# Kernel optimization log

Measured on AMD Instinct MI355X. Metric: run time of the kernel, lower is better.

## Reference

```python
import jax, jax.numpy as jnp
import numpy as np

B, N, D_POINTS, D_MODEL = 2, 65536, 64, 128
SCALE = 1.0 / np.float32(np.sqrt(D_MODEL))


def setup_inputs() -> dict:
    key = jax.random.key(0)
    ks = jax.random.split(key, 20)
    def lin(k, fan_in, fan_out):
        s = 1.0 / np.sqrt(fan_in)
        return jax.random.uniform(k, (fan_in, fan_out), jnp.float32, -s, s)
    return {
        "xyz": jax.random.normal(ks[0], (B, N, 3), jnp.float32),
        "features": jax.random.normal(ks[1], (B, N, D_POINTS), jnp.float32),
        "fc1_w": lin(ks[2], D_POINTS, D_MODEL), "fc1_b": jnp.zeros((D_MODEL,), jnp.float32),
        "fc2_w": lin(ks[3], D_MODEL, D_POINTS), "fc2_b": jnp.zeros((D_POINTS,), jnp.float32),
        "d1_w": lin(ks[4], 3, D_MODEL), "d1_b": jnp.zeros((D_MODEL,), jnp.float32),
        "d2_w": lin(ks[5], D_MODEL, D_MODEL), "d2_b": jnp.zeros((D_MODEL,), jnp.float32),
        "g1_w": lin(ks[6], D_MODEL, D_MODEL), "g1_b": jnp.zeros((D_MODEL,), jnp.float32),
        "g2_w": lin(ks[7], D_MODEL, D_MODEL), "g2_b": jnp.zeros((D_MODEL,), jnp.float32),
        "wq": lin(ks[8], D_MODEL, D_MODEL),
        "wk": lin(ks[9], D_MODEL, D_MODEL),
        "wv": lin(ks[10], D_MODEL, D_MODEL),
    }


def reference(xyz, features, fc1_w, fc1_b, fc2_w, fc2_b, d1_w, d1_b, d2_w, d2_b,
              g1_w, g1_b, g2_w, g2_b, wq, wk, wv):
    # x: [B, N, d_model]
    x = features @ fc1_w + fc1_b
    q = x @ wq
    k = x @ wk
    v = x @ wv
    # position encoding MLP on xyz: [B, N, d_model]
    pos_enc = jax.nn.relu(xyz @ d1_w + d1_b) @ d2_w + d2_b
    # vector attention: elementwise q - k + pos_enc, gamma MLP, per-channel softmax over points
    attn = jax.nn.relu((q - k + pos_enc) @ g1_w + g1_b) @ g2_w + g2_b
    attn = jax.nn.softmax(attn * SCALE, axis=-2)  # softmax over N (point axis)
    # elementwise gating of values
    res = attn * (v + pos_enc)
    res = res @ fc2_w + fc2_b + features  # residual
    return (res, attn)
```

## Files before the change

### kernel.cpp

```cpp
#include <hip/hip_runtime.h>
#include <hip/hip_bf16.h>

#define BB 2
#define NN 65536
#define DP 64
#define DM 128
#define SCALEF 0.08838834764831845f

typedef __attribute__((ext_vector_type(8))) short short8v;
typedef __attribute__((ext_vector_type(4))) float float4v;

__device__ __forceinline__ unsigned short f2bf(float f) {
  unsigned u = __float_as_uint(f);
  u += 0x7FFFu + ((u >> 16) & 1u);
  return (unsigned short)(u >> 16);
}
__device__ __forceinline__ float bf2f(unsigned short h) {
  return __uint_as_float(((unsigned)h) << 16);
}

__global__ __launch_bounds__(256) void k0_kernel(
    const float* __restrict__ wq, const float* __restrict__ wk,
    const float* __restrict__ fc1_w, const float* __restrict__ fc2_w,
    const float* __restrict__ d2_w, const float* __restrict__ g1_w,
    const float* __restrict__ g2_w, const float* __restrict__ wv_w,
    float* __restrict__ sums,
    short* __restrict__ d2t, short* __restrict__ fc1t, short* __restrict__ wqkt,
    short* __restrict__ g1t, short* __restrict__ g2t, short* __restrict__ wvt,
    short* __restrict__ fc2t) {
  int t = threadIdx.x, bi = blockIdx.x;
  if (bi == 0) sums[t] = 0.f;
  int mat = bi >> 5, blk = bi & 31;
  if (mat == 1) {
    int i = blk * 256 + t;
    int n = i >> 6, k = i & 63;
    fc1t[n * 64 + k] = (short)f2bf(fc1_w[k * 128 + n]);
  } else if (mat == 6) {
    int i = blk * 256 + t;
    int n = i >> 7, k = i & 127;
    fc2t[n * 128 + k] = (short)f2bf(fc2_w[k * 64 + n]);
  } else {
    const float* src = (mat == 0) ? d2_w : (mat == 2) ? wq : (mat == 3) ? g1_w
                     : (mat == 4) ? g2_w : wv_w;
    short* dst = (mat == 0) ? d2t : (mat == 2) ? wqkt : (mat == 3) ? g1t
               : (mat == 4) ? g2t : wvt;
#pragma unroll
    for (int j = 0; j < 2; ++j) {
      int i = blk * 512 + t + j * 256;
      int n = i >> 7, k = i & 127;
      float v = src[k * 128 + n];
      if (mat == 2) v -= wk[k * 128 + n];
      dst[n * 128 + k] = (short)f2bf(v);
    }
  }
}

template<int K>
__device__ __forceinline__ void loadB(const short* __restrict__ Wt,
                                      int wid, int col, int quad, short8v b[2][4]) {
#pragma unroll
  for (int nt = 0; nt < 2; ++nt)
#pragma unroll
    for (int kt = 0; kt < K / 32; ++kt)
      b[nt][kt] = *(const short8v*)(Wt + (wid * 32 + nt * 16 + col) * K + kt * 32 + quad * 8);
}

template<int K>
__device__ __forceinline__ void gemm_compute(const short* __restrict__ A,
                                             const short8v b[2][4],
                                             int col, int quad, float4v acc[2][2]) {
#pragma unroll
  for (int kt = 0; kt < K / 32; ++kt) {
#pragma unroll
    for (int mt = 0; mt < 2; ++mt) {
      short8v a = *(const short8v*)(A + (mt * 16 + col) * 136 + kt * 32 + quad * 8);
      acc[mt][0] = __builtin_amdgcn_mfma_f32_16x16x32_bf16(a, b[0][kt], acc[mt][0], 0, 0, 0);
      acc[mt][1] = __builtin_amdgcn_mfma_f32_16x16x32_bf16(a, b[1][kt], acc[mt][1], 0, 0, 0);
    }
  }
}

__device__ __forceinline__ void store_tile(short* __restrict__ dst,
                                           const float4v acc[2][2],
                                           int wid, int col, int quad,
                                           float b0, float b1, bool do_relu) {
#pragma unroll
  for (int mt = 0; mt < 2; ++mt)
#pragma unroll
    for (int nt = 0; nt < 2; ++nt) {
      float bias = nt ? b1 : b0;
#pragma unroll
      for (int r = 0; r < 4; ++r) {
        float v = acc[mt][nt][r] + bias;
        if (do_relu) v = fmaxf(v, 0.f);
        dst[(mt * 16 + quad * 4 + r) * 136 + wid * 32 + nt * 16 + col] = (short)f2bf(v);
      }
    }
}

#define ZERO_ACC(acc) \
  _Pragma("unroll") for (int mt = 0; mt < 2; ++mt) \
  _Pragma("unroll") for (int nt = 0; nt < 2; ++nt) \
  _Pragma("unroll") for (int r = 0; r < 4; ++r) acc[mt][nt][r] = 0.f;

__global__ __launch_bounds__(256, 5) void k1_kernel(
    const float* __restrict__ xyz, const float* __restrict__ features,
    const short* __restrict__ fc1t, const float* __restrict__ fc1_b,
    const float* __restrict__ d1_w, const float* __restrict__ d1_b,
    const short* __restrict__ d2t, const float* __restrict__ d2_b,
    const short* __restrict__ g1t, const float* __restrict__ g1_b,
    const short* __restrict__ g2t, const float* __restrict__ g2_b,
    const short* __restrict__ wqkt, const short* __restrict__ wvt,
    unsigned short* __restrict__ Ebf, unsigned short* __restrict__ Gbf,
    float* __restrict__ sums) {
  __shared__ __align__(16) short As[32 * 136];
  __shared__ __align__(16) short Xs[32 * 136];

  const int tid = threadIdx.x;
  const int wid = tid >> 6, lane = tid & 63;
  const int col = lane & 15, quad = lane >> 4;
  const long long p0 = (long long)blockIdx.x * 32;
  const int bi = (int)(p0 >> 16);

  short8v b[2][4];
  loadB<128>(d2t, wid, col, quad, b);

  float* xf = (float*)Xs;
  if (tid < 96) xf[tid] = xyz[p0 * 3 + tid];
  __syncthreads();

  {
    const int tn = tid & 31, tm = tid >> 5;
    const int c4 = tn * 4, pbase = tm * 4;
    float4 w0 = *(const float4*)(d1_w + c4);
    float4 w1 = *(const float4*)(d1_w + 128 + c4);
    float4 w2 = *(const float4*)(d1_w + 256 + c4);
    float4 bb = *(const float4*)(d1_b + c4);
#pragma unroll
    for (int p = 0; p < 4; ++p) {
      float x0 = xf[(pbase + p) * 3 + 0];
      float x1 = xf[(pbase + p) * 3 + 1];
      float x2 = xf[(pbase + p) * 3 + 2];
      short4 rr;
      rr.x = (short)f2bf(fmaxf(0.f, fmaf(x0, w0.x, fmaf(x1, w1.x, fmaf(x2, w2.x, bb.x)))));
      rr.y = (short)f2bf(fmaxf(0.f, fmaf(x0, w0.y, fmaf(x1, w1.y, fmaf(x2, w2.y, bb.y)))));
      rr.z = (short)f2bf(fmaxf(0.f, fmaf(x0, w0.z, fmaf(x1, w1.z, fmaf(x2, w2.z, bb.z)))));
      rr.w = (short)f2bf(fmaxf(0.f, fmaf(x0, w0.w, fmaf(x1, w1.w, fmaf(x2, w2.w, bb.w)))));
      *(short4*)(As + (pbase + p) * 136 + c4) = rr;
    }
  }
  __syncthreads();

  const int ch0 = wid * 32 + col, ch1 = ch0 + 16;
  float4v pe[2][2], acc[2][2];

  ZERO_ACC(acc)
  gemm_compute<128>(As, b, col, quad, acc);
  {
    float b0 = d2_b[ch0], b1 = d2_b[ch1];
#pragma unroll
    for (int mt = 0; mt < 2; ++mt)
#pragma unroll
      for (int r = 0; r < 4; ++r) {
        pe[mt][0][r] = acc[mt][0][r] + b0;
        pe[mt][1][r] = acc[mt][1][r] + b1;
      }
  }
  loadB<64>(fc1t, wid, col, quad, b);
  __syncthreads();

#pragma unroll
  for (int j = 0; j < 2; ++j) {
    int c = tid + j * 256;
    float4 f = *(const float4*)(features + p0 * 64 + (long long)c * 4);
    int row = c >> 4, cp = (c & 15) * 4;
    short4 s;
    s.x = (short)f2bf(f.x); s.y = (short)f2bf(f.y);
    s.z = (short)f2bf(f.z); s.w = (short)f2bf(f.w);
    *(short4*)(As + row * 136 + cp) = s;
  }
  __syncthreads();

  ZERO_ACC(acc)
  gemm_compute<64>(As, b, col, quad, acc);
  store_tile(Xs, acc, wid, col, quad, fc1_b[ch0], fc1_b[ch1], false);
  loadB<128>(wqkt, wid, col, quad, b);
  __syncthreads();

#pragma unroll
  for (int mt = 0; mt < 2; ++mt)
#pragma unroll
    for (int nt = 0; nt < 2; ++nt)
#pragma unroll
      for (int r = 0; r < 4; ++r) acc[mt][nt][r] = pe[mt][nt][r];
  gemm_compute<128>(Xs, b, col, quad, acc);
  store_tile(As, acc, wid, col, quad, 0.f, 0.f, false);
  loadB<128>(g1t, wid, col, quad, b);
  __syncthreads();

  ZERO_ACC(acc)
  gemm_compute<128>(As, b, col, quad, acc);
  __syncthreads();
  store_tile(As, acc, wid, col, quad, g1_b[ch0], g1_b[ch1], true);
  loadB<128>(g2t, wid, col, quad, b);
  __syncthreads();

  ZERO_ACC(acc)
  gemm_compute<128>(As, b, col, quad, acc);
  {
    short8v b2[2][4];
    loadB<128>(wvt, wid, col, quad, b2);
    float b0 = g2_b[ch0], b1 = g2_b[ch1];
    float s0 = 0.f, s1 = 0.f;
#pragma unroll
    for (int mt = 0; mt < 2; ++mt)
#pragma unroll
      for (int r = 0; r < 4; ++r) {
        long long row = p0 + mt * 16 + quad * 4 + r;
        float e0 = __expf((acc[mt][0][r] + b0) * SCALEF);
        float e1 = __expf((acc[mt][1][r] + b1) * SCALEF);
        Ebf[row * DM + ch0] = f2bf(e0);
        Ebf[row * DM + ch1] = f2bf(e1);
        s0 += e0; s1 += e1;
      }
    s0 += __shfl_xor(s0, 16, 64); s0 += __shfl_xor(s0, 32, 64);
    s1 += __shfl_xor(s1, 16, 64); s1 += __shfl_xor(s1, 32, 64);
    if (quad == 0) {
      atomicAdd(&sums[bi * DM + ch0], s0);
      atomicAdd(&sums[bi * DM + ch1], s1);
    }

#pragma unroll
    for (int mt = 0; mt < 2; ++mt)
#pragma unroll
      for (int nt = 0; nt < 2; ++nt)
#pragma unroll
        for (int r = 0; r < 4; ++r) acc[mt][nt][r] = pe[mt][nt][r];
    gemm_compute<128>(Xs, b2, col, quad, acc);
#pragma unroll
    for (int mt = 0; mt < 2; ++mt)
#pragma unroll
      for (int r = 0; r < 4; ++r) {
        long long row = p0 + mt * 16 + quad * 4 + r;
        Gbf[row * DM + ch0] = f2bf(acc[mt][0][r]);
        Gbf[row * DM + ch1] = f2bf(acc[mt][1][r]);
      }
  }
}

__global__ __launch_bounds__(256, 5) void k3_kernel(
    const unsigned short* __restrict__ Ebf, float* __restrict__ out_attn,
    float* __restrict__ out_res, const unsigned short* __restrict__ Gbf,
    const float* __restrict__ sums,
    const short* __restrict__ fc2t, const float* __restrict__ fc2_b,
    const float* __restrict__ features) {
  __shared__ __align__(16) short Ys[32 * 136];
  const int tid = threadIdx.x;
  const long long p0 = (long long)blockIdx.x * 32;
  const int bi = (int)(p0 >> 16);

  {
    const int tn = tid & 15, tm = tid >> 4;
    const int c8 = tn * 8;
    float4 sv0 = *(const float4*)(sums + bi * DM + c8);
    float4 sv1 = *(const float4*)(sums + bi * DM + c8 + 4);
    float4 r0, r1;
    r0.x = 1.f / sv0.x; r0.y = 1.f / sv0.y; r0.z = 1.f / sv0.z; r0.w = 1.f / sv0.w;
    r1.x = 1.f / sv1.x; r1.y = 1.f / sv1.y; r1.z = 1.f / sv1.z; r1.w = 1.f / sv1.w;
#pragma unroll
    for (int it = 0; it < 2; ++it) {
      int row = tm + it * 16;
      long long idx = (p0 + row) * DM + c8;
      short8v e8 = *(const short8v*)(Ebf + idx);
      short8v g8 = *(const short8v*)(Gbf + idx);
      float a[8];
      a[0] = bf2f((unsigned short)e8[0]) * r0.x; a[1] = bf2f((unsigned short)e8[1]) * r0.y;
      a[2] = bf2f((unsigned short)e8[2]) * r0.z; a[3] = bf2f((unsigned short)e8[3]) * r0.w;
      a[4] = bf2f((unsigned short)e8[4]) * r1.x; a[5] = bf2f((unsigned short)e8[5]) * r1.y;
      a[6] = bf2f((unsigned short)e8[6]) * r1.z; a[7] = bf2f((unsigned short)e8[7]) * r1.w;
      float4 a0 = {a[0], a[1], a[2], a[3]};
      float4 a1 = {a[4], a[5], a[6], a[7]};
      *(float4*)(out_attn + idx) = a0;
      *(float4*)(out_attn + idx + 4) = a1;
      short8v y;
#pragma unroll
      for (int q = 0; q < 8; ++q)
        y[q] = (short)f2bf(a[q] * bf2f((unsigned short)g8[q]));
      *(short8v*)(Ys + row * 136 + c8) = y;
    }
  }

  const int wid = tid >> 6, lane = tid & 63;
  const int col = lane & 15, quad = lane >> 4;
  const int n = wid * 16 + col;
  short8v bw[4];
#pragma unroll
  for (int kt = 0; kt < 4; ++kt)
    bw[kt] = *(const short8v*)(fc2t + n * DM + kt * 32 + quad * 8);
  __syncthreads();

  float4v acc[2];
#pragma unroll
  for (int mt = 0; mt < 2; ++mt)
#pragma unroll
    for (int r = 0; r < 4; ++r) acc[mt][r] = 0.f;
#pragma unroll
  for (int kt = 0; kt < 4; ++kt)
#pragma unroll
    for (int mt = 0; mt < 2; ++mt) {
      short8v a = *(const short8v*)(Ys + (mt * 16 + col) * 136 + kt * 32 + quad * 8);
      acc[mt] = __builtin_amdgcn_mfma_f32_16x16x32_bf16(a, bw[kt], acc[mt], 0, 0, 0);
    }
  __syncthreads();
  float* yf = (float*)Ys;
  float bb = fc2_b[n];
#pragma unroll
  for (int mt = 0; mt < 2; ++mt)
#pragma unroll
    for (int r = 0; r < 4; ++r)
      yf[(mt * 16 + quad * 4 + r) * 68 + n] = acc[mt][r] + bb;
  __syncthreads();

#pragma unroll
  for (int it = 0; it < 2; ++it) {
    int idx = tid + it * 256;
    int row = idx >> 4, ch = idx & 15;
    float4 v = *(const float4*)(yf + row * 68 + ch * 4);
    float4 ft = *(const float4*)(features + (p0 + row) * DP + ch * 4);
    float4 o;
    o.x = v.x + ft.x; o.y = v.y + ft.y; o.z = v.z + ft.z; o.w = v.w + ft.w;
    *(float4*)(out_res + (p0 + row) * DP + ch * 4) = o;
  }
}

extern "C" void kernel_launch(void* const* d_in, const int* in_sizes, int n_in,
                              void* d_out, int out_size, void* d_ws, size_t ws_size,
                              hipStream_t stream) {
  const float* xyz      = (const float*)d_in[0];
  const float* features = (const float*)d_in[1];
  const float* fc1_w    = (const float*)d_in[2];
  const float* fc1_b    = (const float*)d_in[3];
  const float* fc2_w    = (const float*)d_in[4];
  const float* fc2_b    = (const float*)d_in[5];
  const float* d1_w     = (const float*)d_in[6];
  const float* d1_b     = (const float*)d_in[7];
  const float* d2_w     = (const float*)d_in[8];
  const float* d2_b     = (const float*)d_in[9];
  const float* g1_w     = (const float*)d_in[10];
  const float* g1_b     = (const float*)d_in[11];
  const float* g2_w     = (const float*)d_in[12];
  const float* g2_b     = (const float*)d_in[13];
  const float* wq       = (const float*)d_in[14];
  const float* wk       = (const float*)d_in[15];
  const float* wv       = (const float*)d_in[16];

  float* out_res  = (float*)d_out;
  float* out_attn = out_res + (long long)BB * NN * DP;

  float* sums = (float*)d_ws;
  short* d2t  = (short*)(sums + 256);
  short* fc1t = d2t + 16384;
  short* wqkt = fc1t + 8192;
  short* g1t  = wqkt + 16384;
  short* g2t  = g1t + 16384;
  short* wvt  = g2t + 16384;
  short* fc2t = wvt + 16384;
  unsigned short* Ebf = (unsigned short*)(fc2t + 8192);
  unsigned short* Gbf = (unsigned short*)d_out;

  hipLaunchKernelGGL(k0_kernel, dim3(224), dim3(256), 0, stream,
                     wq, wk, fc1_w, fc2_w, d2_w, g1_w, g2_w, wv,
                     sums, d2t, fc1t, wqkt, g1t, g2t, wvt, fc2t);
  hipLaunchKernelGGL(k1_kernel, dim3((BB * NN) / 32), dim3(256), 0, stream,
                     xyz, features, fc1t, fc1_b, d1_w, d1_b, d2t, d2_b,
                     g1t, g1_b, g2t, g2_b, wqkt, wvt, Ebf, Gbf, sums);
  hipLaunchKernelGGL(k3_kernel, dim3((BB * NN) / 32), dim3(256), 0, stream,
                     Ebf, out_attn, out_res, Gbf, sums, fc2t, fc2_b, features);
}
```

Measured before the change: 283.9 us.

## Make k1/k3 persistent with register-resident weights and batched softmax-sum atomics

Both point-wise kernels go from one 32-point tile per block to 512 blocks that each loop over 8 consecutive tiles. All B-operand weight fragments, biases and softmax reciprocals are loaded once per block and kept in registers, and the softmax partial sums are accumulated across iterations so atomics happen once per block. Global loads of features and xyz are issued at the top of each iteration ahead of the barriers to overlap latency. The cost is much higher register pressure (five 128x128 weight fragment sets held at once, launch bounds lowered to 2) and only 512 blocks, which may limit occupancy and latency hiding on a 256-CU part.

```diff
diff --git a/kernel.cpp b/kernel.cpp
--- a/kernel.cpp
+++ b/kernel.cpp
@@ -9,6 +9,11 @@
 
 typedef __attribute__((ext_vector_type(8))) short short8v;
 typedef __attribute__((ext_vector_type(4))) float float4v;
+
+#define K1_GRID 512
+#define K1_ITERS 8
+#define K3_GRID 512
+#define K3_ITERS 8
 
 __device__ __forceinline__ unsigned short f2bf(float f) {
   unsigned u = __float_as_uint(f);
@@ -103,7 +108,12 @@
   _Pragma("unroll") for (int nt = 0; nt < 2; ++nt) \
   _Pragma("unroll") for (int r = 0; r < 4; ++r) acc[mt][nt][r] = 0.f;
 
-__global__ __launch_bounds__(256, 5) void k1_kernel(
+#define COPY_ACC(dst, src) \
+  _Pragma("unroll") for (int mt = 0; mt < 2; ++mt) \
+  _Pragma("unroll") for (int nt = 0; nt < 2; ++nt) \
+  _Pragma("unroll") for (int r = 0; r < 4; ++r) dst[mt][nt][r] = src[mt][nt][r];
+
+__global__ __launch_bounds__(256, 2) void k1_kernel(
     const float* __restrict__ xyz, const float* __restrict__ features,
     const short* __restrict__ fc1t, const float* __restrict__ fc1_b,
     const float* __restrict__ d1_w, const float* __restrict__ d1_b,
@@ -119,124 +129,119 @@
   const int tid = threadIdx.x;
   const int wid = tid >> 6, lane = tid & 63;
   const int col = lane & 15, quad = lane >> 4;
-  const long long p0 = (long long)blockIdx.x * 32;
-  const int bi = (int)(p0 >> 16);
-
-  short8v b[2][4];
-  loadB<128>(d2t, wid, col, quad, b);
-
+  const int bk = blockIdx.x;
+  const int bi = bk >> 8;
+  const int ch0 = wid * 32 + col, ch1 = ch0 + 16;
+
+  short8v Bd2[2][4], Bqk[2][4], Bg1[2][4], Bg2[2][4], Bwv[2][4];
+  loadB<128>(d2t, wid, col, quad, Bd2);
+  loadB<128>(wqkt, wid, col, quad, Bqk);
+  loadB<128>(g1t, wid, col, quad, Bg1);
+  loadB<128>(g2t, wid, col, quad, Bg2);
+  loadB<128>(wvt, wid, col, quad, Bwv);
+
+  const float d2b0 = d2_b[ch0], d2b1 = d2_b[ch1];
+  const float f1b0 = fc1_b[ch0], f1b1 = fc1_b[ch1];
+  const float g1b0 = g1_b[ch0], g1b1 = g1_b[ch1];
+  const float g2b0 = g2_b[ch0], g2b1 = g2_b[ch1];
+
+  float s0 = 0.f, s1 = 0.f;
   float* xf = (float*)Xs;
-  if (tid < 96) xf[tid] = xyz[p0 * 3 + tid];
-  __syncthreads();
-
-  {
-    const int tn = tid & 31, tm = tid >> 5;
-    const int c4 = tn * 4, pbase = tm * 4;
-    float4 w0 = *(const float4*)(d1_w + c4);
-    float4 w1 = *(const float4*)(d1_w + 128 + c4);
-    float4 w2 = *(const float4*)(d1_w + 256 + c4);
-    float4 bb = *(const float4*)(d1_b + c4);
-#pragma unroll
-    for (int p = 0; p < 4; ++p) {
-      float x0 = xf[(pbase + p) * 3 + 0];
-      float x1 = xf[(pbase + p) * 3 + 1];
-      float x2 = xf[(pbase + p) * 3 + 2];
-      short4 rr;
-      rr.x = (short)f2bf(fmaxf(0.f, fmaf(x0, w0.x, fmaf(x1, w1.x, fmaf(x2, w2.x, bb.x)))));
-      rr.y = (short)f2bf(fmaxf(0.f, fmaf(x0, w0.y, fmaf(x1, w1.y, fmaf(x2, w2.y, bb.y)))));
-      rr.z = (short)f2bf(fmaxf(0.f, fmaf(x0, w0.z, fmaf(x1, w1.z, fmaf(x2, w2.z, bb.z)))));
-      rr.w = (short)f2bf(fmaxf(0.f, fmaf(x0, w0.w, fmaf(x1, w1.w, fmaf(x2, w2.w, bb.w)))));
-      *(short4*)(As + (pbase + p) * 136 + c4) = rr;
-    }
-  }
-  __syncthreads();
-
-  const int ch0 = wid * 32 + col, ch1 = ch0 + 16;
-  float4v pe[2][2], acc[2][2];
-
-  ZERO_ACC(acc)
-  gemm_compute<128>(As, b, col, quad, acc);
-  {
-    float b0 = d2_b[ch0], b1 = d2_b[ch1];
+
+  for (int it = 0; it < K1_ITERS; ++it) {
+    const long long p0 = ((long long)bk * K1_ITERS + it) * 32;
+
+    float xr = 0.f;
+    if (tid < 96) xr = xyz[p0 * 3 + tid];
+    float4 f0 = *(const float4*)(features + p0 * 64 + (long long)tid * 4);
+    float4 f1 = *(const float4*)(features + p0 * 64 + (long long)(tid + 256) * 4);
+    short8v Bf1[2][4];
+    loadB<64>(fc1t, wid, col, quad, Bf1);
+
+    __syncthreads();
+    if (tid < 96) xf[tid] = xr;
+    __syncthreads();
+
+    {
+      const int tn = tid & 31, tm = tid >> 5;
+      const int c4 = tn * 4, pbase = tm * 4;
+      float4 w0 = *(const float4*)(d1_w + c4);
+      float4 w1 = *(const float4*)(d1_w + 128 + c4);
+      float4 w2 = *(const float4*)(d1_w + 256 + c4);
+      float4 bb = *(const float4*)(d1_b + c4);
+#pragma unroll
+      for (int p = 0; p < 4; ++p) {
+        float x0 = xf[(pbase + p) * 3 + 0];
+        float x1 = xf[(pbase + p) * 3 + 1];
+        float x2 = xf[(pbase + p) * 3 + 2];
+        short4 rr;
+        rr.x = (short)f2bf(fmaxf(0.f, fmaf(x0, w0.x, fmaf(x1, w1.x, fmaf(x2, w2.x, bb.x)))));
+        rr.y = (short)f2bf(fmaxf(0.f, fmaf(x0, w0.y, fmaf(x1, w1.y, fmaf(x2, w2.y, bb.y)))));
+        rr.z = (short)f2bf(fmaxf(0.f, fmaf(x0, w0.z, fmaf(x1, w1.z, fmaf(x2, w2.z, bb.z)))));
+        rr.w = (short)f2bf(fmaxf(0.f, fmaf(x0, w0.w, fmaf(x1, w1.w, fmaf(x2, w2.w, bb.w)))));
+        *(short4*)(As + (pbase + p) * 136 + c4) = rr;
+      }
+    }
+    __syncthreads();
+
+    float4v pe[2][2], acc[2][2];
+
+    ZERO_ACC(acc)
+    gemm_compute<128>(As, Bd2, col, quad, acc);
 #pragma unroll
     for (int mt = 0; mt < 2; ++mt)
 #pragma unroll
       for (int r = 0; r < 4; ++r) {
-        pe[mt][0][r] = acc[mt][0][r] + b0;
-        pe[mt][1][r] = acc[mt][1][r] + b1;
-      }
-  }
-  loadB<64>(fc1t, wid, col, quad, b);
-  __syncthreads();
-
-#pragma unroll
-  for (int j = 0; j < 2; ++j) {
-    int c = tid + j * 256;
-    float4 f = *(const float4*)(features + p0 * 64 + (long long)c * 4);
-    int row = c >> 4, cp = (c & 15) * 4;
-    short4 s;
-    s.x = (short)f2bf(f.x); s.y = (short)f2bf(f.y);
-    s.z = (short)f2bf(f.z); s.w = (short)f2bf(f.w);
-    *(short4*)(As + row * 136 + cp) = s;
-  }
-  __syncthreads();
-
-  ZERO_ACC(acc)
-  gemm_compute<64>(As, b, col, quad, acc);
-  store_tile(Xs, acc, wid, col, quad, fc1_b[ch0], fc1_b[ch1], false);
-  loadB<128>(wqkt, wid, col, quad, b);
-  __syncthreads();
-
-#pragma unroll
-  for (int mt = 0; mt < 2; ++mt)
-#pragma unroll
-    for (int nt = 0; nt < 2; ++nt)
-#pragma unroll
-      for (int r = 0; r < 4; ++r) acc[mt][nt][r] = pe[mt][nt][r];
-  gemm_compute<128>(Xs, b, col, quad, acc);
-  store_tile(As, acc, wid, col, quad, 0.f, 0.f, false);
-  loadB<128>(g1t, wid, col, quad, b);
-  __syncthreads();
-
-  ZERO_ACC(acc)
-  gemm_compute<128>(As, b, col, quad, acc);
-  __syncthreads();
-  store_tile(As, acc, wid, col, quad, g1_b[ch0], g1_b[ch1], true);
-  loadB<128>(g2t, wid, col, quad, b);
-  __syncthreads();
-
-  ZERO_ACC(acc)
-  gemm_compute<128>(As, b, col, quad, acc);
-  {
-    short8v b2[2][4];
-    loadB<128>(wvt, wid, col, quad, b2);
-    float b0 = g2_b[ch0], b1 = g2_b[ch1];
-    float s0 = 0.f, s1 = 0.f;
+        pe[mt][0][r] = acc[mt][0][r] + d2b0;
+        pe[mt][1][r] = acc[mt][1][r] + d2b1;
+      }
+    __syncthreads();
+
+    {
+      int c = tid, row = c >> 4, cp = (c & 15) * 4;
+      short4 s;
+      s.x = (short)f2bf(f0.x); s.y = (short)f2bf(f0.y);
+      s.z = (short)f2bf(f0.z); s.w = (short)f2bf(f0.w);
+      *(short4*)(As + row * 136 + cp) = s;
+      c = tid + 256; row = c >> 4; cp = (c & 15) * 4;
+      s.x = (short)f2bf(f1.x); s.y = (short)f2bf(f1.y);
+      s.z = (short)f2bf(f1.z); s.w = (short)f2bf(f1.w);
+      *(short4*)(As + row * 136 + cp) = s;
+    }
+    __syncthreads();
+
+    ZERO_ACC(acc)
+    gemm_compute<64>(As, Bf1, col, quad, acc);
+    store_tile(Xs, acc, wid, col, quad, f1b0, f1b1, false);
+    __syncthreads();
+
+    COPY_ACC(acc, pe)
+    gemm_compute<128>(Xs, Bqk, col, quad, acc);
+    store_tile(As, acc, wid, col, quad, 0.f, 0.f, false);
+    __syncthreads();
+
+    ZERO_ACC(acc)
+    gemm_compute<128>(As, Bg1, col, quad, acc);
+    __syncthreads();
+    store_tile(As, acc, wid, col, quad, g1b0, g1b1, true);
+    __syncthreads();
+
+    ZERO_ACC(acc)
+    gemm_compute<128>(As, Bg2, col, quad, acc);
 #pragma unroll
     for (int mt = 0; mt < 2; ++mt)
 #pragma unroll
       for (int r = 0; r < 4; ++r) {
         long long row = p0 + mt * 16 + quad * 4 + r;
-        float e0 = __expf((acc[mt][0][r] + b0) * SCALEF);
-        float e1 = __expf((acc[mt][1][r] + b1) * SCALEF);
+        float e0 = __expf((acc[mt][0][r] + g2b0) * SCALEF);
+        float e1 = __expf((acc[mt][1][r] + g2b1) * SCALEF);
         Ebf[row * DM + ch0] = f2bf(e0);
         Ebf[row * DM + ch1] = f2bf(e1);
         s0 += e0; s1 += e1;
       }
-    s0 += __shfl_xor(s0, 16, 64); s0 += __shfl_xor(s0, 32, 64);
-    s1 += __shfl_xor(s1, 16, 64); s1 += __shfl_xor(s1, 32, 64);
-    if (quad == 0) {
-      atomicAdd(&sums[bi * DM + ch0], s0);
-      atomicAdd(&sums[bi * DM + ch1], s1);
-    }
-
-#pragma unroll
-    for (int mt = 0; mt < 2; ++mt)
-#pragma unroll
-      for (int nt = 0; nt < 2; ++nt)
-#pragma unroll
-        for (int r = 0; r < 4; ++r) acc[mt][nt][r] = pe[mt][nt][r];
-    gemm_compute<128>(Xs, b2, col, quad, acc);
+
+    COPY_ACC(acc, pe)
+    gemm_compute<128>(Xs, Bwv, col, quad, acc);
 #pragma unroll
     for (int mt = 0; mt < 2; ++mt)
 #pragma unroll
@@ -246,9 +251,16 @@
         Gbf[row * DM + ch1] = f2bf(acc[mt][1][r]);
       }
   }
-}
-
-__global__ __launch_bounds__(256, 5) void k3_kernel(
+
+  s0 += __shfl_xor(s0, 16, 64); s0 += __shfl_xor(s0, 32, 64);
+  s1 += __shfl_xor(s1, 16, 64); s1 += __shfl_xor(s1, 32, 64);
+  if (quad == 0) {
+    atomicAdd(&sums[bi * DM + ch0], s0);
+    atomicAdd(&sums[bi * DM + ch1], s1);
+  }
+}
+
+__global__ __launch_bounds__(256, 2) void k3_kernel(
     const unsigned short* __restrict__ Ebf, float* __restrict__ out_attn,
     float* __restrict__ out_res, const unsigned short* __restrict__ Gbf,
     const float* __restrict__ sums,
@@ -256,20 +268,39 @@
     const float* __restrict__ features) {
   __shared__ __align__(16) short Ys[32 * 136];
   const int tid = threadIdx.x;
-  const long long p0 = (long long)blockIdx.x * 32;
-  const int bi = (int)(p0 >> 16);
-
-  {
-    const int tn = tid & 15, tm = tid >> 4;
-    const int c8 = tn * 8;
-    float4 sv0 = *(const float4*)(sums + bi * DM + c8);
-    float4 sv1 = *(const float4*)(sums + bi * DM + c8 + 4);
-    float4 r0, r1;
-    r0.x = 1.f / sv0.x; r0.y = 1.f / sv0.y; r0.z = 1.f / sv0.z; r0.w = 1.f / sv0.w;
-    r1.x = 1.f / sv1.x; r1.y = 1.f / sv1.y; r1.z = 1.f / sv1.z; r1.w = 1.f / sv1.w;
-#pragma unroll
-    for (int it = 0; it < 2; ++it) {
-      int row = tm + it * 16;
+  const int bk = blockIdx.x;
+  const int bi = bk >> 8;
+
+  const int wid = tid >> 6, lane = tid & 63;
+  const int col = lane & 15, quad = lane >> 4;
+  const int n = wid * 16 + col;
+  short8v bw[4];
+#pragma unroll
+  for (int kt = 0; kt < 4; ++kt)
+    bw[kt] = *(const short8v*)(fc2t + n * DM + kt * 32 + quad * 8);
+  const float bb = fc2_b[n];
+
+  const int tn = tid & 15, tm = tid >> 4;
+  const int c8 = tn * 8;
+  float4 sv0 = *(const float4*)(sums + bi * DM + c8);
+  float4 sv1 = *(const float4*)(sums + bi * DM + c8 + 4);
+  float4 r0, r1;
+  r0.x = 1.f / sv0.x; r0.y = 1.f / sv0.y; r0.z = 1.f / sv0.z; r0.w = 1.f / sv0.w;
+  r1.x = 1.f / sv1.x; r1.y = 1.f / sv1.y; r1.z = 1.f / sv1.z; r1.w = 1.f / sv1.w;
+
+  for (int it = 0; it < K3_ITERS; ++it) {
+    const long long p0 = ((long long)bk * K3_ITERS + it) * 32;
+
+    int fidx = tid, frow = fidx >> 4, fch = fidx & 15;
+    float4 ft0 = *(const float4*)(features + (p0 + frow) * DP + fch * 4);
+    int fidx1 = tid + 256, frow1 = fidx1 >> 4, fch1 = fidx1 & 15;
+    float4 ft1 = *(const float4*)(features + (p0 + frow1) * DP + fch1 * 4);
+
+    __syncthreads();
+
+#pragma unroll
+    for (int it2 = 0; it2 < 2; ++it2) {
+      int row = tm + it2 * 16;
       long long idx = (p0 + row) * DM + c8;
       short8v e8 = *(const short8v*)(Ebf + idx);
       short8v g8 = *(const short8v*)(Gbf + idx);
@@ -288,48 +319,38 @@
         y[q] = (short)f2bf(a[q] * bf2f((unsigned short)g8[q]));
       *(short8v*)(Ys + row * 136 + c8) = y;
     }
-  }
-
-  const int wid = tid >> 6, lane = tid & 63;
-  const int col = lane & 15, quad = lane >> 4;
-  const int n = wid * 16 + col;
-  short8v bw[4];
-#pragma unroll
-  for (int kt = 0; kt < 4; ++kt)
-    bw[kt] = *(const short8v*)(fc2t + n * DM + kt * 32 + quad * 8);
-  __syncthreads();
-
-  float4v acc[2];
-#pragma unroll
-  for (int mt = 0; mt < 2; ++mt)
-#pragma unroll
-    for (int r = 0; r < 4; ++r) acc[mt][r] = 0.f;
-#pragma unroll
-  for (int kt = 0; kt < 4; ++kt)
-#pragma unroll
-    for (int mt = 0; mt < 2; ++mt) {
-      short8v a = *(const short8v*)(Ys + (mt * 16 + col) * 136 + kt * 32 + quad * 8);
-      acc[mt] = __builtin_amdgcn_mfma_f32_16x16x32_bf16(a, bw[kt], acc[mt], 0, 0, 0);
-    }
-  __syncthreads();
-  float* yf = (float*)Ys;
-  float bb = fc2_b[n];
-#pragma unroll
-  for (int mt = 0; mt < 2; ++mt)
-#pragma unroll
-    for (int r = 0; r < 4; ++r)
-      yf[(mt * 16 + quad * 4 + r) * 68 + n] = acc[mt][r] + bb;
-  __syncthreads();
-
-#pragma unroll
-  for (int it = 0; it < 2; ++it) {
-    int idx = tid + it * 256;
-    int row = idx >> 4, ch = idx & 15;
-    float4 v = *(const float4*)(yf + row * 68 + ch * 4);
-    float4 ft = *(const float4*)(features + (p0 + row) * DP + ch * 4);
-    float4 o;
-    o.x = v.x + ft.x; o.y = v.y + ft.y; o.z = v.z + ft.z; o.w = v.w + ft.w;
-    *(float4*)(out_res + (p0 + row) * DP + ch * 4) = o;
+    __syncthreads();
+
+    float4v acc[2];
+#pragma unroll
+    for (int mt = 0; mt < 2; ++mt)
+#pragma unroll
+      for (int r = 0; r < 4; ++r) acc[mt][r] = 0.f;
+#pragma unroll
+    for (int kt = 0; kt < 4; ++kt)
+#pragma unroll
+      for (int mt = 0; mt < 2; ++mt) {
+        short8v a = *(const short8v*)(Ys + (mt * 16 + col) * 136 + kt * 32 + quad * 8);
+        acc[mt] = __builtin_amdgcn_mfma_f32_16x16x32_bf16(a, bw[kt], acc[mt], 0, 0, 0);
+      }
+    __syncthreads();
+    float* yf = (float*)Ys;
+#pragma unroll
+    for (int mt = 0; mt < 2; ++mt)
+#pragma unroll
+      for (int r = 0; r < 4; ++r)
+        yf[(mt * 16 + quad * 4 + r) * 68 + n] = acc[mt][r] + bb;
+    __syncthreads();
+
+    {
+      float4 v = *(const float4*)(yf + frow * 68 + fch * 4);
+      float4 o;
+      o.x = v.x + ft0.x; o.y = v.y + ft0.y; o.z = v.z + ft0.z; o.w = v.w + ft0.w;
+      *(float4*)(out_res + (p0 + frow) * DP + fch * 4) = o;
+      v = *(const float4*)(yf + frow1 * 68 + fch1 * 4);
+      o.x = v.x + ft1.x; o.y = v.y + ft1.y; o.z = v.z + ft1.z; o.w = v.w + ft1.w;
+      *(float4*)(out_res + (p0 + frow1) * DP + fch1 * 4) = o;
+    }
   }
 }
 
@@ -371,9 +392,9 @@
   hipLaunchKernelGGL(k0_kernel, dim3(224), dim3(256), 0, stream,
                      wq, wk, fc1_w, fc2_w, d2_w, g1_w, g2_w, wv,
                      sums, d2t, fc1t, wqkt, g1t, g2t, wvt, fc2t);
-  hipLaunchKernelGGL(k1_kernel, dim3((BB * NN) / 32), dim3(256), 0, stream,
+  hipLaunchKernelGGL(k1_kernel, dim3(K1_GRID), dim3(256), 0, stream,
                      xyz, features, fc1t, fc1_b, d1_w, d1_b, d2t, d2_b,
                      g1t, g1_b, g2t, g2_b, wqkt, wvt, Ebf, Gbf, sums);
-  hipLaunchKernelGGL(k3_kernel, dim3((BB * NN) / 32), dim3(256), 0, stream,
+  hipLaunchKernelGGL(k3_kernel, dim3(K3_GRID), dim3(256), 0, stream,
                      Ebf, out_attn, out_res, Gbf, sums, fc2t, fc2_b, features);
 }
```

Result: faster. 234.1 us (-17.5%).
